# Optimization experiments

Measured on AMD Instinct MI355X. Metric: run time of the kernel, lower is better.

The kernel has to match this reference:

```python
import jax, jax.numpy as jnp
import numpy as np

NUM_GRAPHS = 1024

def setup_inputs() -> dict:
    key = jax.random.key(0)
    k1, k2, k3, k4 = jax.random.split(key, 4)
    N, D, H = 200000, 512, 128
    h = jax.random.normal(k1, (N, D), dtype=jnp.float32)
    batch = jnp.sort(jax.random.randint(k2, (N,), 0, NUM_GRAPHS)).astype(jnp.int32)
    # gate MLP params: Linear(D,H) -> tanh -> Linear(H,1)
    W1 = jax.random.normal(k3, (D, H), dtype=jnp.float32) / np.sqrt(D)
    b1 = jnp.zeros((H,), dtype=jnp.float32)
    W2 = jax.random.normal(k4, (H, 1), dtype=jnp.float32) / np.sqrt(H)
    b2 = jnp.zeros((1,), dtype=jnp.float32)
    return {"h": h, "batch": batch, "W1": W1, "b1": b1, "W2": W2, "b2": b2}

def reference(h, batch, W1, b1, W2, b2):
    # gate MLP -> per-node logit
    logits = (jnp.tanh(h @ W1 + b1) @ W2 + b2)[:, 0]  # [N]
    # segment softmax over nodes within each graph
    seg_max = jax.ops.segment_max(logits, batch, num_segments=NUM_GRAPHS,
                                  indices_are_sorted=True)  # [G]
    ex = jnp.exp(logits - seg_max[batch])  # [N]
    denom = jax.ops.segment_sum(ex, batch, num_segments=NUM_GRAPHS,
                                indices_are_sorted=True)  # [G]
    a = ex / denom[batch]  # [N]
    # weighted scatter-add pooling
    pooled = jax.ops.segment_sum(h * a[:, None], batch, num_segments=NUM_GRAPHS,
                                 indices_are_sorted=True)  # [G, D]
    return pooled
```

## Files before the change

kernel.cpp:

```cpp
#include <hip/hip_runtime.h>
#include <hip/hip_bf16.h>

typedef __attribute__((ext_vector_type(8))) short short8;
typedef __attribute__((ext_vector_type(4))) float f32x4;

#define NGRAPHS 1024
#define D_DIM 512
#define H_DIM 128
#define BM 64

static __device__ __forceinline__ unsigned int pack_bf2(float a, float b) {
    float2 t; t.x = a; t.y = b;
    __hip_bfloat162 h = __float22bfloat162_rn(t);
    union { __hip_bfloat162 h; unsigned int u; } v;
    v.h = h;
    return v.u;
}

static __device__ __forceinline__ unsigned short f2bf(float f) {
    __hip_bfloat16 h = __float2bfloat16(f);
    union { __hip_bfloat16 h; unsigned short u; } v;
    v.h = h;
    return v.u;
}

static __device__ __forceinline__ float fast_tanh(float x) {
    float cx = fminf(fmaxf(x, -15.f), 15.f);
    float e = __expf(2.f * cx);
    return (e - 1.f) / (e + 1.f);
}

__global__ void seg_offsets_kernel(const int* __restrict__ batch, int N,
                                   int* __restrict__ off) {
    int g = blockIdx.x * 256 + threadIdx.x;
    if (g > NGRAPHS) return;
    int lo = 0, hi = N;
    while (lo < hi) {
        int mid = (lo + hi) >> 1;
        if (batch[mid] < g) lo = mid + 1;
        else hi = mid;
    }
    off[g] = lo;
}

__global__ void prep_w1t_kernel(const float* __restrict__ W1,
                                unsigned short* __restrict__ W1TF) {
    int idx = blockIdx.x * 256 + threadIdx.x;
    int e = idx & 7;
    int lane = (idx >> 3) & 63;
    int ki = (idx >> 9) & 15;
    int cgrp = idx >> 13;
    int col = cgrp * 16 + (lane & 15);
    int k = ki * 32 + (lane >> 4) * 8 + e;
    W1TF[idx] = f2bf(W1[k * H_DIM + col]);
}

__global__ __launch_bounds__(512) void gate_pool_partial_kernel(
    const float* __restrict__ h, const unsigned short* __restrict__ W1TF,
    const float* __restrict__ b1, const float* __restrict__ W2,
    const int* __restrict__ batch, float* __restrict__ P,
    float* __restrict__ out, int N) {
    __shared__ unsigned short hA[BM * D_DIM];
    __shared__ float plds[8][BM];
    __shared__ float wl[BM];
    __shared__ int gb[BM];

    const int tid = threadIdx.x;
    const int lane = tid & 63;
    const int w = tid >> 6;
    const int cg = lane & 15;
    const int qg = lane >> 4;
    const int row0 = blockIdx.x * BM;

    if (tid < BM) {
        int gr = row0 + tid;
        gb[tid] = batch[gr < N ? gr : N - 1];
    }

#pragma unroll
    for (int b4 = 0; b4 < 4; ++b4) {
        float4 f[4];
#pragma unroll
        for (int i = 0; i < 4; ++i) {
            const int t = (b4 * 4 + i) * 8 + w;
            const int row = t >> 1, half = t & 1;
            int gr = row0 + row;
            gr = gr < N ? gr : N - 1;
            f[i] = *(const float4*)(h + (size_t)gr * D_DIM + half * 256 + lane * 4);
        }
#pragma unroll
        for (int i = 0; i < 4; ++i) {
            const int t = (b4 * 4 + i) * 8 + w;
            const int row = t >> 1, half = t & 1;
            const int unit = half * 32 + (lane >> 1);
            uint2 v;
            v.x = pack_bf2(f[i].x, f[i].y);
            v.y = pack_bf2(f[i].z, f[i].w);
            *(uint2*)&hA[row * 512 + ((unit ^ (row & 7)) * 8) + (lane & 1) * 4] = v;
        }
    }

    short8 bfr[16];
#pragma unroll
    for (int ki = 0; ki < 16; ++ki)
        bfr[ki] = *(const short8*)(W1TF + (((w * 16 + ki) << 9)) + lane * 8);
    __syncthreads();

    f32x4 acc[4];
#pragma unroll
    for (int rf = 0; rf < 4; ++rf) acc[rf] = (f32x4){0.f, 0.f, 0.f, 0.f};
#pragma unroll
    for (int ki = 0; ki < 16; ++ki) {
#pragma unroll
        for (int rf = 0; rf < 4; ++rf) {
            const short8 af = *(const short8*)&hA[(rf * 16 + cg) * 512 +
                (((4 * ki + qg) ^ (cg & 7)) * 8)];
            acc[rf] = __builtin_amdgcn_mfma_f32_16x16x32_bf16(af, bfr[ki],
                                                              acc[rf], 0, 0, 0);
        }
    }

    const float b1v = b1[w * 16 + cg];
    const float w2v = W2[w * 16 + cg];
#pragma unroll
    for (int rf = 0; rf < 4; ++rf) {
#pragma unroll
        for (int reg = 0; reg < 4; ++reg) {
            float p = fast_tanh(acc[rf][reg] + b1v) * w2v;
#pragma unroll
            for (int o = 1; o < 16; o <<= 1) p += __shfl_xor(p, o, 64);
            if (cg == 0) plds[w][rf * 16 + qg * 4 + reg] = p;
        }
    }
    __syncthreads();

    if (tid < BM) {
        float l = plds[0][tid] + plds[1][tid] + plds[2][tid] + plds[3][tid] +
                  plds[4][tid] + plds[5][tid] + plds[6][tid] + plds[7][tid];
        wl[tid] = (row0 + tid < N) ? __expf(fminf(l, 60.f)) : 0.f;
    }
    __syncthreads();

    if (tid < 256) {
        const int d0 = (tid >> 2) * 8 + (tid & 3) * 2;
        float ax = 0.f, ay = 0.f, d = 0.f;
        int cur = gb[0];
#pragma unroll 8
        for (int j = 0; j < BM; ++j) {
            const int gj = gb[j];
            if (gj != cur) {
                if (cur == gb[0]) {
                    float* rec = P + (size_t)blockIdx.x * 2 * 513;
                    rec[d0] = ax; rec[d0 + 1] = ay;
                    if (tid == 0) rec[512] = d;
                } else {
                    out[(size_t)cur * D_DIM + d0] = ax / d;
                    out[(size_t)cur * D_DIM + d0 + 1] = ay / d;
                }
                ax = 0.f; ay = 0.f; d = 0.f; cur = gj;
            }
            const float wj = wl[j];
            const unsigned int pair = *(const unsigned int*)&hA[j * 512 +
                (((tid >> 2) ^ (j & 7)) * 8) + (tid & 3) * 2];
            ax += wj * __uint_as_float(pair << 16);
            ay += wj * __uint_as_float(pair & 0xffff0000u);
            d += wj;
        }
        {
            const int slot = (cur == gb[0]) ? 0 : 1;
            float* rec = P + ((size_t)blockIdx.x * 2 + slot) * 513;
            rec[d0] = ax; rec[d0 + 1] = ay;
            if (tid == 0) rec[512] = d;
        }
        if (gb[0] == gb[BM - 1]) {
            float* r1 = P + ((size_t)blockIdx.x * 2 + 1) * 513;
            r1[d0] = 0.f; r1[d0 + 1] = 0.f;
            if (tid == 0) r1[512] = 0.f;
        }
    }
}

__global__ __launch_bounds__(512) void reduce_kernel(
    const float* __restrict__ P, const int* __restrict__ off,
    const int* __restrict__ batch, float* __restrict__ out, int N) {
    const int g = blockIdx.x;
    const int tid = threadIdx.x;
    const int s = off[g], e = off[g + 1];
    if (e <= s) { out[(size_t)g * D_DIM + tid] = 0.f; return; }
    const int b0 = s >> 6, b1 = (e - 1) >> 6;
    float sum = 0.f, den = 0.f;
    bool found = false;
    for (int b = b0; b <= b1; ++b) {
        const int fg = batch[b << 6];
        const int le = (b << 6) + 63;
        const int lg = batch[le < N ? le : N - 1];
        if (fg == g) {
            const float* rec = P + (size_t)b * 2 * 513;
            sum += rec[tid]; den += rec[512]; found = true;
        } else if (lg == g) {
            const float* rec = P + ((size_t)b * 2 + 1) * 513;
            sum += rec[tid]; den += rec[512]; found = true;
        }
    }
    if (found) out[(size_t)g * D_DIM + tid] = sum / den;
}

__global__ void zero_kernel(float* __restrict__ out, float* __restrict__ den) {
    int i = blockIdx.x * 256 + threadIdx.x;
    if (i < NGRAPHS * D_DIM) out[i] = 0.f;
    if (i < NGRAPHS) den[i] = 0.f;
}

__global__ __launch_bounds__(256) void gate_pool_atomic_kernel(
    const float* __restrict__ h, const unsigned short* __restrict__ W1TF,
    const float* __restrict__ b1, const float* __restrict__ W2,
    const int* __restrict__ batch, float* __restrict__ outnum,
    float* __restrict__ den, int N) {
    __shared__ unsigned short hA[BM * D_DIM];
    __shared__ float plds[4][BM];
    __shared__ float wl[BM];
    __shared__ int gb[BM];

    const int tid = threadIdx.x;
    const int lane = tid & 63;
    const int w = tid >> 6;
    const int cg = lane & 15;
    const int qg = lane >> 4;
    const int row0 = blockIdx.x * BM;

    if (tid < BM) {
        int gr = row0 + tid;
        gb[tid] = batch[gr < N ? gr : N - 1];
    }
#pragma unroll
    for (int b = 0; b < 4; ++b) {
        float4 fa[4], fb[4];
#pragma unroll
        for (int i = 0; i < 4; ++i) {
            const int fi = (b * 4 + i) * 256 + tid;
            const int r = fi >> 6, u = fi & 63;
            int gr = row0 + r;
            gr = gr < N ? gr : N - 1;
            const float* p = h + (size_t)gr * D_DIM + u * 8;
            fa[i] = *(const float4*)p;
            fb[i] = *(const float4*)(p + 4);
        }
#pragma unroll
        for (int i = 0; i < 4; ++i) {
            const int fi = (b * 4 + i) * 256 + tid;
            const int r = fi >> 6, u = fi & 63;
            uint4 val;
            val.x = pack_bf2(fa[i].x, fa[i].y);
            val.y = pack_bf2(fa[i].z, fa[i].w);
            val.z = pack_bf2(fb[i].x, fb[i].y);
            val.w = pack_bf2(fb[i].z, fb[i].w);
            *(uint4*)&hA[r * D_DIM + ((u ^ (r & 7)) * 8)] = val;
        }
    }
    __syncthreads();

    f32x4 acc[4][2];
#pragma unroll
    for (int rf = 0; rf < 4; ++rf)
#pragma unroll
        for (int cf = 0; cf < 2; ++cf) acc[rf][cf] = (f32x4){0.f, 0.f, 0.f, 0.f};
#pragma unroll
    for (int ki = 0; ki < 16; ++ki) {
        short8 bfg[2];
#pragma unroll
        for (int cf = 0; cf < 2; ++cf)
            bfg[cf] = *(const short8*)(W1TF + (((w * 2 + cf) * 16 + ki) << 9) + lane * 8);
#pragma unroll
        for (int rf = 0; rf < 4; ++rf) {
            const int row = rf * 16 + cg;
            const short8 af = *(const short8*)&hA[row * D_DIM +
                (((4 * ki + qg) ^ (row & 7)) * 8)];
#pragma unroll
            for (int cf = 0; cf < 2; ++cf)
                acc[rf][cf] = __builtin_amdgcn_mfma_f32_16x16x32_bf16(
                    af, bfg[cf], acc[rf][cf], 0, 0, 0);
        }
    }
    const float b1v0 = b1[w * 32 + cg];
    const float b1v1 = b1[w * 32 + 16 + cg];
    const float w2v0 = W2[w * 32 + cg];
    const float w2v1 = W2[w * 32 + 16 + cg];
#pragma unroll
    for (int rf = 0; rf < 4; ++rf) {
#pragma unroll
        for (int reg = 0; reg < 4; ++reg) {
            float p = fast_tanh(acc[rf][0][reg] + b1v0) * w2v0 +
                      fast_tanh(acc[rf][1][reg] + b1v1) * w2v1;
#pragma unroll
            for (int o = 1; o < 16; o <<= 1) p += __shfl_xor(p, o, 64);
            if (cg == 0) plds[w][rf * 16 + qg * 4 + reg] = p;
        }
    }
    __syncthreads();
    if (tid < BM) {
        const float l = plds[0][tid] + plds[1][tid] + plds[2][tid] + plds[3][tid];
        wl[tid] = (row0 + tid < N) ? __expf(fminf(l, 60.f)) : 0.f;
    }
    __syncthreads();

    const int d0 = (tid >> 2) * 8 + (tid & 3) * 2;
    float ax = 0.f, ay = 0.f;
    int cur = gb[0];
#pragma unroll 8
    for (int j = 0; j < BM; ++j) {
        const int gj = gb[j];
        if (gj != cur) {
            atomicAdd(&outnum[(size_t)cur * D_DIM + d0], ax);
            atomicAdd(&outnum[(size_t)cur * D_DIM + d0 + 1], ay);
            ax = 0.f; ay = 0.f; cur = gj;
        }
        const float wj = wl[j];
        const unsigned int pair = *(const unsigned int*)&hA[j * D_DIM +
            (((tid >> 2) ^ (j & 7)) * 8) + (tid & 3) * 2];
        ax += wj * __uint_as_float(pair << 16);
        ay += wj * __uint_as_float(pair & 0xffff0000u);
    }
    atomicAdd(&outnum[(size_t)cur * D_DIM + d0], ax);
    atomicAdd(&outnum[(size_t)cur * D_DIM + d0 + 1], ay);

    if (tid == 0) {
        float a = 0.f;
        int c2 = gb[0];
        for (int j = 0; j < BM; ++j) {
            if (gb[j] != c2) { atomicAdd(&den[c2], a); a = 0.f; c2 = gb[j]; }
            a += wl[j];
        }
        atomicAdd(&den[c2], a);
    }
}

__global__ __launch_bounds__(512) void finalize_kernel(
    float* __restrict__ out, const float* __restrict__ den) {
    const int g = blockIdx.x;
    const float dv = den[g];
    const float v = out[(size_t)g * D_DIM + threadIdx.x];
    out[(size_t)g * D_DIM + threadIdx.x] = dv > 0.f ? v / dv : 0.f;
}

extern "C" void kernel_launch(void* const* d_in, const int* in_sizes, int n_in,
                              void* d_out, int out_size, void* d_ws, size_t ws_size,
                              hipStream_t stream) {
    const float* h = (const float*)d_in[0];
    const int* batch = (const int*)d_in[1];
    const float* W1 = (const float*)d_in[2];
    const float* b1 = (const float*)d_in[3];
    const float* W2 = (const float*)d_in[4];
    float* out = (float*)d_out;
    const int N = in_sizes[1];
    const int NB = (N + BM - 1) / BM;

    char* ws = (char*)d_ws;
    int* off = (int*)ws;
    unsigned short* W1TF = (unsigned short*)(ws + 4608);
    float* P = (float*)(ws + 135680);

    const size_t need = 135680 + (size_t)NB * 2 * 513 * 4;

    seg_offsets_kernel<<<(NGRAPHS + 256) / 256 + 1, 256, 0, stream>>>(batch, N, off);
    prep_w1t_kernel<<<(D_DIM * H_DIM) / 256, 256, 0, stream>>>(W1, W1TF);

    if (ws_size >= need) {
        gate_pool_partial_kernel<<<NB, 512, 0, stream>>>(h, W1TF, b1, W2, batch,
                                                         P, out, N);
        reduce_kernel<<<NGRAPHS, 512, 0, stream>>>(P, off, batch, out, N);
    } else {
        float* den = P;
        zero_kernel<<<(NGRAPHS * D_DIM + 255) / 256, 256, 0, stream>>>(out, den);
        gate_pool_atomic_kernel<<<NB, 256, 0, stream>>>(h, W1TF, b1, W2, batch,
                                                        out, den, N);
        finalize_kernel<<<NGRAPHS, 512, 0, stream>>>(out, den);
    }
}
```

Before: 150.8 us.

## Make gate-pool kernel persistent with double-buffered LDS prefetch of next tile

Replaces the one-block-per-64-row-tile gate/pool kernel with a persistent kernel of 256 blocks that loop over tiles. While each tile runs its MFMA and pooling, the next tile's h rows are loaded into registers and written to a second LDS buffer, so global loads overlap with compute. W1 fragments are also loaded once per block instead of once per tile. In exchange LDS use doubles to about 130 KB per block, 64 extra registers hold the prefetch, and only 256 blocks of 512 threads are launched, so each CU runs at most one block and there may be too few waves to hide memory latency.

Result: slower. 278.8 us (+84.8%).

```diff
diff --git a/kernel.cpp b/kernel.cpp
--- a/kernel.cpp
+++ b/kernel.cpp
@@ -8,6 +8,7 @@
 #define D_DIM 512
 #define H_DIM 128
 #define BM 64
+#define PBLK 256
 
 static __device__ __forceinline__ unsigned int pack_bf2(float a, float b) {
     float2 t; t.x = a; t.y = b;
@@ -55,12 +56,40 @@
     W1TF[idx] = f2bf(W1[k * H_DIM + col]);
 }
 
-__global__ __launch_bounds__(512) void gate_pool_partial_kernel(
+static __device__ __forceinline__ void stage_issue(const float* __restrict__ h,
+                                                   int N, int t, int w, int lane,
+                                                   float4* f) {
+#pragma unroll
+    for (int i = 0; i < 16; ++i) {
+        const int task = i * 8 + w;
+        const int row = task >> 1, half = task & 1;
+        int gr = t * BM + row;
+        gr = gr < N ? gr : N - 1;
+        f[i] = *(const float4*)(h + (size_t)gr * D_DIM + half * 256 + lane * 4);
+    }
+}
+
+static __device__ __forceinline__ void stage_commit(unsigned short* __restrict__ buf,
+                                                    int w, int lane,
+                                                    const float4* f) {
+#pragma unroll
+    for (int i = 0; i < 16; ++i) {
+        const int task = i * 8 + w;
+        const int row = task >> 1, half = task & 1;
+        const int unit = half * 32 + (lane >> 1);
+        uint2 v;
+        v.x = pack_bf2(f[i].x, f[i].y);
+        v.y = pack_bf2(f[i].z, f[i].w);
+        *(uint2*)&buf[row * D_DIM + ((unit ^ (row & 7)) * 8) + (lane & 1) * 4] = v;
+    }
+}
+
+__global__ __launch_bounds__(512, 2) void gate_pool_persist_kernel(
     const float* __restrict__ h, const unsigned short* __restrict__ W1TF,
     const float* __restrict__ b1, const float* __restrict__ W2,
     const int* __restrict__ batch, float* __restrict__ P,
-    float* __restrict__ out, int N) {
-    __shared__ unsigned short hA[BM * D_DIM];
+    float* __restrict__ out, int N, int NT) {
+    __shared__ unsigned short hA[2][BM * D_DIM];
     __shared__ float plds[8][BM];
     __shared__ float wl[BM];
     __shared__ int gb[BM];
@@ -70,113 +99,110 @@
     const int w = tid >> 6;
     const int cg = lane & 15;
     const int qg = lane >> 4;
-    const int row0 = blockIdx.x * BM;
-
-    if (tid < BM) {
-        int gr = row0 + tid;
-        gb[tid] = batch[gr < N ? gr : N - 1];
-    }
-
-#pragma unroll
-    for (int b4 = 0; b4 < 4; ++b4) {
-        float4 f[4];
-#pragma unroll
-        for (int i = 0; i < 4; ++i) {
-            const int t = (b4 * 4 + i) * 8 + w;
-            const int row = t >> 1, half = t & 1;
-            int gr = row0 + row;
-            gr = gr < N ? gr : N - 1;
-            f[i] = *(const float4*)(h + (size_t)gr * D_DIM + half * 256 + lane * 4);
-        }
-#pragma unroll
-        for (int i = 0; i < 4; ++i) {
-            const int t = (b4 * 4 + i) * 8 + w;
-            const int row = t >> 1, half = t & 1;
-            const int unit = half * 32 + (lane >> 1);
-            uint2 v;
-            v.x = pack_bf2(f[i].x, f[i].y);
-            v.y = pack_bf2(f[i].z, f[i].w);
-            *(uint2*)&hA[row * 512 + ((unit ^ (row & 7)) * 8) + (lane & 1) * 4] = v;
-        }
-    }
 
     short8 bfr[16];
 #pragma unroll
     for (int ki = 0; ki < 16; ++ki)
-        bfr[ki] = *(const short8*)(W1TF + (((w * 16 + ki) << 9)) + lane * 8);
-    __syncthreads();
-
-    f32x4 acc[4];
-#pragma unroll
-    for (int rf = 0; rf < 4; ++rf) acc[rf] = (f32x4){0.f, 0.f, 0.f, 0.f};
-#pragma unroll
-    for (int ki = 0; ki < 16; ++ki) {
-#pragma unroll
-        for (int rf = 0; rf < 4; ++rf) {
-            const short8 af = *(const short8*)&hA[(rf * 16 + cg) * 512 +
-                (((4 * ki + qg) ^ (cg & 7)) * 8)];
-            acc[rf] = __builtin_amdgcn_mfma_f32_16x16x32_bf16(af, bfr[ki],
-                                                              acc[rf], 0, 0, 0);
-        }
-    }
+        bfr[ki] = *(const short8*)(W1TF + ((w * 16 + ki) << 9) + lane * 8);
 
     const float b1v = b1[w * 16 + cg];
     const float w2v = W2[w * 16 + cg];
-#pragma unroll
-    for (int rf = 0; rf < 4; ++rf) {
-#pragma unroll
-        for (int reg = 0; reg < 4; ++reg) {
-            float p = fast_tanh(acc[rf][reg] + b1v) * w2v;
-#pragma unroll
-            for (int o = 1; o < 16; o <<= 1) p += __shfl_xor(p, o, 64);
-            if (cg == 0) plds[w][rf * 16 + qg * 4 + reg] = p;
-        }
+    const int d0 = (tid >> 2) * 8 + (tid & 3) * 2;
+
+    int t = blockIdx.x;
+    if (t >= NT) return;
+    {
+        float4 f[16];
+        stage_issue(h, N, t, w, lane, f);
+        stage_commit(&hA[0][0], w, lane, f);
     }
     __syncthreads();
 
-    if (tid < BM) {
-        float l = plds[0][tid] + plds[1][tid] + plds[2][tid] + plds[3][tid] +
-                  plds[4][tid] + plds[5][tid] + plds[6][tid] + plds[7][tid];
-        wl[tid] = (row0 + tid < N) ? __expf(fminf(l, 60.f)) : 0.f;
-    }
-    __syncthreads();
-
-    if (tid < 256) {
-        const int d0 = (tid >> 2) * 8 + (tid & 3) * 2;
-        float ax = 0.f, ay = 0.f, d = 0.f;
-        int cur = gb[0];
+    int cur = 0;
+    for (;;) {
+        if (tid < BM) {
+            int gr = t * BM + tid;
+            gb[tid] = batch[gr < N ? gr : N - 1];
+        }
+        const int tn = t + PBLK;
+        const bool have = tn < NT;
+        float4 pf[16];
+        if (have) stage_issue(h, N, tn, w, lane, pf);
+        __builtin_amdgcn_sched_barrier(0);
+
+        f32x4 acc[4];
+#pragma unroll
+        for (int rf = 0; rf < 4; ++rf) acc[rf] = (f32x4){0.f, 0.f, 0.f, 0.f};
+#pragma unroll
+        for (int ki = 0; ki < 16; ++ki) {
+#pragma unroll
+            for (int rf = 0; rf < 4; ++rf) {
+                const short8 af = *(const short8*)&hA[cur][(rf * 16 + cg) * D_DIM +
+                    (((4 * ki + qg) ^ (cg & 7)) * 8)];
+                acc[rf] = __builtin_amdgcn_mfma_f32_16x16x32_bf16(af, bfr[ki],
+                                                                  acc[rf], 0, 0, 0);
+            }
+        }
+
+#pragma unroll
+        for (int rf = 0; rf < 4; ++rf) {
+#pragma unroll
+            for (int reg = 0; reg < 4; ++reg) {
+                float p = fast_tanh(acc[rf][reg] + b1v) * w2v;
+#pragma unroll
+                for (int o = 1; o < 16; o <<= 1) p += __shfl_xor(p, o, 64);
+                if (cg == 0) plds[w][rf * 16 + qg * 4 + reg] = p;
+            }
+        }
+        __syncthreads();
+
+        if (tid < BM) {
+            float l = plds[0][tid] + plds[1][tid] + plds[2][tid] + plds[3][tid] +
+                      plds[4][tid] + plds[5][tid] + plds[6][tid] + plds[7][tid];
+            wl[tid] = (t * BM + tid < N) ? __expf(fminf(l, 60.f)) : 0.f;
+        }
+        __syncthreads();
+
+        if (tid < 256) {
+            float ax = 0.f, ay = 0.f, d = 0.f;
+            int curg = gb[0];
 #pragma unroll 8
-        for (int j = 0; j < BM; ++j) {
-            const int gj = gb[j];
-            if (gj != cur) {
-                if (cur == gb[0]) {
-                    float* rec = P + (size_t)blockIdx.x * 2 * 513;
-                    rec[d0] = ax; rec[d0 + 1] = ay;
-                    if (tid == 0) rec[512] = d;
-                } else {
-                    out[(size_t)cur * D_DIM + d0] = ax / d;
-                    out[(size_t)cur * D_DIM + d0 + 1] = ay / d;
+            for (int j = 0; j < BM; ++j) {
+                const int gj = gb[j];
+                if (gj != curg) {
+                    if (curg == gb[0]) {
+                        float* rec = P + (size_t)t * 2 * 513;
+                        rec[d0] = ax; rec[d0 + 1] = ay;
+                        if (tid == 0) rec[512] = d;
+                    } else {
+                        out[(size_t)curg * D_DIM + d0] = ax / d;
+                        out[(size_t)curg * D_DIM + d0 + 1] = ay / d;
+                    }
+                    ax = 0.f; ay = 0.f; d = 0.f; curg = gj;
                 }
-                ax = 0.f; ay = 0.f; d = 0.f; cur = gj;
+                const float wj = wl[j];
+                const unsigned int pair = *(const unsigned int*)&hA[cur][j * D_DIM +
+                    (((tid >> 2) ^ (j & 7)) * 8) + (tid & 3) * 2];
+                ax += wj * __uint_as_float(pair << 16);
+                ay += wj * __uint_as_float(pair & 0xffff0000u);
+                d += wj;
             }
-            const float wj = wl[j];
-            const unsigned int pair = *(const unsigned int*)&hA[j * 512 +
-                (((tid >> 2) ^ (j & 7)) * 8) + (tid & 3) * 2];
-            ax += wj * __uint_as_float(pair << 16);
-            ay += wj * __uint_as_float(pair & 0xffff0000u);
-            d += wj;
-        }
-        {
-            const int slot = (cur == gb[0]) ? 0 : 1;
-            float* rec = P + ((size_t)blockIdx.x * 2 + slot) * 513;
+            const int slot = (curg == gb[0]) ? 0 : 1;
+            float* rec = P + ((size_t)t * 2 + slot) * 513;
             rec[d0] = ax; rec[d0 + 1] = ay;
             if (tid == 0) rec[512] = d;
-        }
-        if (gb[0] == gb[BM - 1]) {
-            float* r1 = P + ((size_t)blockIdx.x * 2 + 1) * 513;
-            r1[d0] = 0.f; r1[d0 + 1] = 0.f;
-            if (tid == 0) r1[512] = 0.f;
-        }
+            if (gb[0] == gb[BM - 1]) {
+                float* r1 = P + ((size_t)t * 2 + 1) * 513;
+                r1[d0] = 0.f; r1[d0 + 1] = 0.f;
+                if (tid == 0) r1[512] = 0.f;
+            }
+        }
+
+        if (have) stage_commit(&hA[cur ^ 1][0], w, lane, pf);
+        __syncthreads();
+        if (!have) break;
+        t = tn;
+        cur ^= 1;
     }
 }
 
@@ -187,10 +213,10 @@
     const int tid = threadIdx.x;
     const int s = off[g], e = off[g + 1];
     if (e <= s) { out[(size_t)g * D_DIM + tid] = 0.f; return; }
-    const int b0 = s >> 6, b1 = (e - 1) >> 6;
+    const int t0 = s >> 6, t1 = (e - 1) >> 6;
     float sum = 0.f, den = 0.f;
     bool found = false;
-    for (int b = b0; b <= b1; ++b) {
+    for (int b = t0; b <= t1; ++b) {
         const int fg = batch[b << 6];
         const int le = (b << 6) + 63;
         const int lg = batch[le < N ? le : N - 1];
@@ -352,26 +378,26 @@
     const float* W2 = (const float*)d_in[4];
     float* out = (float*)d_out;
     const int N = in_sizes[1];
-    const int NB = (N + BM - 1) / BM;
+    const int NT = (N + BM - 1) / BM;
 
     char* ws = (char*)d_ws;
     int* off = (int*)ws;
     unsigned short* W1TF = (unsigned short*)(ws + 4608);
     float* P = (float*)(ws + 135680);
 
-    const size_t need = 135680 + (size_t)NB * 2 * 513 * 4;
+    const size_t need = 135680 + (size_t)NT * 2 * 513 * 4;
 
     seg_offsets_kernel<<<(NGRAPHS + 256) / 256 + 1, 256, 0, stream>>>(batch, N, off);
     prep_w1t_kernel<<<(D_DIM * H_DIM) / 256, 256, 0, stream>>>(W1, W1TF);
 
     if (ws_size >= need) {
-        gate_pool_partial_kernel<<<NB, 512, 0, stream>>>(h, W1TF, b1, W2, batch,
-                                                         P, out, N);
+        gate_pool_persist_kernel<<<PBLK, 512, 0, stream>>>(h, W1TF, b1, W2, batch,
+                                                           P, out, N, NT);
         reduce_kernel<<<NGRAPHS, 512, 0, stream>>>(P, off, batch, out, N);
     } else {
         float* den = P;
         zero_kernel<<<(NGRAPHS * D_DIM + 255) / 256, 256, 0, stream>>>(out, den);
-        gate_pool_atomic_kernel<<<NB, 256, 0, stream>>>(h, W1TF, b1, W2, batch,
+        gate_pool_atomic_kernel<<<NT, 256, 0, stream>>>(h, W1TF, b1, W2, batch,
                                                         out, den, N);
         finalize_kernel<<<NGRAPHS, 512, 0, stream>>>(out, den);
     }
```
